# Performance work log

Hardware: AMD Instinct MI355X
Metric: run time of the kernel (lower is better)

The kernel has to match this reference:

```python
import jax, jax.numpy as jnp
import numpy as np

N_UP, N_DOWN, M, D, K, F, L, B = 16, 16, 4, 128, 64, 32, 3, 1024
N = N_UP + N_DOWN
H_W = 45  # round(sqrt(F*K)), hidden dim of the 2-layer w MLP
LOG2 = float(np.log(2.0))


def ssp(x):
    # shifted softplus activation used by deepqmc
    return jax.nn.softplus(x) - LOG2


def _pair_blocks(n_up, n_down):
    # replicate idx_perm(N,2) grouped by i, then idx_pair_spin partition
    n = n_up + n_down
    i = np.repeat(np.arange(n), n - 1)
    j = np.concatenate([np.concatenate([np.arange(k), np.arange(k + 1, n)]) for k in range(n)])
    blocks = []
    for mi, mj, ri, rj in [(True, True, n_up, max(n_up - 1, 0)),
                           (True, False, n_up, n_down),
                           (False, True, n_down, n_up),
                           (False, False, n_down, max(n_down - 1, 0))]:
        mask = ((i < n_up) == mi) & ((j < n_up) == mj)
        blocks.append((i[mask].reshape(ri, rj), j[mask].reshape(ri, rj)))
    return blocks

_BLOCKS = _pair_blocks(N_UP, N_DOWN)
_CHANS = [0, 1, 1, 0]  # same, anti, anti, same (w/g channel index; 2 = nuclear)


def setup_inputs() -> dict:
    key = jax.random.key(0)
    ks = jax.random.split(key, 12)
    s = 0.1
    return {
        'edges_elec': jax.random.normal(ks[0], (B, N, N, F), jnp.float32),
        'edges_nuc': jax.random.normal(ks[1], (B, N, M, F), jnp.float32),
        'X': jax.random.normal(ks[2], (1, D), jnp.float32) * s,
        'Y': jax.random.normal(ks[3], (M, K), jnp.float32) * s,
        'wW1': jax.random.normal(ks[4], (L, 3, H_W, F), jnp.float32) * s,
        'wb1': jax.random.normal(ks[5], (L, 3, H_W), jnp.float32) * s,
        'wW2': jax.random.normal(ks[6], (L, 3, K, H_W), jnp.float32) * s,
        'wb2': jax.random.normal(ks[7], (L, 3, K), jnp.float32) * s,
        'hW': jax.random.normal(ks[8], (L, K, D), jnp.float32) * s,
        'hb': jax.random.normal(ks[9], (L, K), jnp.float32) * s,
        'gW': jax.random.normal(ks[10], (L, 3, D, K), jnp.float32) * s,
        'gb': jax.random.normal(ks[11], (L, 3, D), jnp.float32) * s,
    }


def reference(edges_elec, edges_nuc, X, Y, wW1, wb1, wW2, wb2, hW, hb, gW, gb):
    def w_mlp(l, c, e):
        # 2-layer log-dim MLP: F -> H_W -> K with SSP in between
        return ssp(e @ wW1[l, c].T + wb1[l, c]) @ wW2[l, c].T + wb2[l, c]

    b = edges_nuc.shape[0]
    x = jnp.broadcast_to(X, (b, N, D))  # initial electron embeddings (n_up==n_down)
    for l in range(L):
        h = x @ hW[l].T + hb[l]  # shared h subnet: [b,N,K]
        zs = []
        for (ii, jj), c in zip(_BLOCKS, _CHANS):
            e = edges_elec[:, ii, jj, :]               # [b, ri, rj, F] gather
            msg = w_mlp(l, c, e) * h[:, jj, :]          # [b, ri, rj, K]
            zs.append(msg.sum(axis=-2))                 # segment-sum over j
        z_same = jnp.concatenate([zs[0], zs[3]], axis=-2)  # up then down
        z_anti = jnp.concatenate([zs[1], zs[2]], axis=-2)
        z_nuc = jnp.einsum('bnmk,mk->bnk', w_mlp(l, 2, edges_nuc), Y)
        update = (z_same @ gW[l, 0].T + gb[l, 0]
                  + z_anti @ gW[l, 1].T + gb[l, 1]
                  + z_nuc @ gW[l, 2].T + gb[l, 2])
        x = x + update  # resnet
    return x
```

## Files before the change

kernel.cpp:

```cpp
#include <hip/hip_runtime.h>
#include <math.h>

#define N_   32
#define NUP_ 16
#define M_   4
#define D_   128
#define K_   64
#define F_   32
#define H_   45
#define L_   3
#define LOG2_ 0.69314718055994530942f

typedef __attribute__((ext_vector_type(8))) short short8;
typedef __attribute__((ext_vector_type(4))) float float4v;

__device__ __forceinline__ float ssp(float v) {
    return __logf(1.0f + __expf(v)) - LOG2_;
}

__device__ __forceinline__ unsigned short f2bf(float x) {
    unsigned int u = __float_as_uint(x);
    return (unsigned short)((u + 0x7FFFu + ((u >> 16) & 1u)) >> 16);
}

__device__ __forceinline__ unsigned int pkbf(float x, float y) {
    return __builtin_amdgcn_perm(__float_as_uint(y) + 0x8000u,
                                 __float_as_uint(x) + 0x8000u, 0x07060302u);
}

__global__ __launch_bounds__(256) void prep_kernel(
    const float* __restrict__ wW1, const float* __restrict__ wb2_unused,
    const float* __restrict__ wW2, const float* __restrict__ wb2,
    const float* __restrict__ gW,  const float* __restrict__ hW,
    const float* __restrict__ gb,
    short* __restrict__ w1B, short* __restrict__ w2B,
    short* __restrict__ gB,  short* __restrict__ hB, float* __restrict__ gbs)
{
    int blk = blockIdx.x;
    int t = threadIdx.x;
    if (blk < 27) {
        int lc = blk / 3, nt = blk % 3;
        short* dst = w1B + (size_t)blk * 512;
        for (int idx = t; idx < 512; idx += 256) {
            int lane = idx >> 3, jj = idx & 7;
            int k = ((lane >> 4) << 3) + jj;
            int n = nt * 16 + (lane & 15);
            float v = (n < H_) ? wW1[((size_t)lc * H_ + n) * F_ + k] : 0.0f;
            dst[idx] = (short)f2bf(v);
        }
    } else if (blk < 99) {
        int b3 = blk - 27;
        int lc = b3 >> 3, rem = b3 & 7, ks = rem >> 2, nt = rem & 3;
        short* dst = w2B + (size_t)b3 * 512;
        for (int idx = t; idx < 512; idx += 256) {
            int lane = idx >> 3, jj = idx & 7;
            int p = ks * 32 + ((lane >> 4) << 3) + jj;
            int n = nt * 16 + (lane & 15);
            float v;
            if (p == 3) v = wb2[(size_t)lc * K_ + n];
            else if ((p & 3) < 3) {
                int u = (p & 3) * 16 + (p >> 2);
                v = (u < H_) ? wW2[((size_t)lc * K_ + n) * H_ + u] : 0.0f;
            } else v = 0.0f;
            dst[idx] = (short)f2bf(v);
        }
    } else if (blk < 243) {
        int g = blk - 99;
        int l = g / 48, rem = g % 48;
        short* dst = gB + (size_t)g * 512;
        for (int idx = t; idx < 512; idx += 256) {
            int lane = idx >> 3, jj = idx & 7;
            int k = (rem >> 3) * 32 + ((lane >> 4) << 3) + jj;
            int c = k >> 6, kk = k & 63;
            int n = ((rem & 7) * 16) + (lane & 15);
            dst[idx] = (short)f2bf(gW[(((size_t)l * 3 + c) * D_ + n) * K_ + kk]);
        }
    } else if (blk < 275) {
        int hh = blk - 243;
        int li = hh >> 4, rem = hh & 15;
        short* dst = hB + (size_t)hh * 512;
        for (int idx = t; idx < 512; idx += 256) {
            int lane = idx >> 3, jj = idx & 7;
            int p = (rem >> 2) * 32 + ((lane >> 4) << 3) + jj;
            int d = (p & 7) * 16 + (p >> 3);
            int n = ((rem & 3) * 16) + (lane & 15);
            dst[idx] = (short)f2bf(hW[(((size_t)(li + 1)) * K_ + n) * D_ + d]);
        }
    } else {
        for (int idx = t; idx < 384; idx += 256) {
            int l = idx >> 7, d = idx & 127;
            gbs[idx] = gb[((size_t)l * 3 + 0) * D_ + d]
                     + gb[((size_t)l * 3 + 1) * D_ + d]
                     + gb[((size_t)l * 3 + 2) * D_ + d];
        }
    }
}

__global__ __launch_bounds__(64) void h0_kernel(
    const float* __restrict__ X, const float* __restrict__ hW,
    const float* __restrict__ hb, float* __restrict__ h0)
{
    int k = threadIdx.x;
    float a = hb[k];
    const float* w = hW + (size_t)k * D_;
    #pragma unroll 8
    for (int dd = 0; dd < D_; ++dd) a += w[dd] * X[dd];
    h0[k] = a;
}

#define WSTRIDE 68
#define HDS 72
__global__ __launch_bounds__(256, 6) void edge_kernel(
    const float* __restrict__ ee, const float* __restrict__ en,
    const float* __restrict__ Y,
    const short* __restrict__ w1B, const float* __restrict__ wb1,
    const short* __restrict__ w2B,
    const float* __restrict__ h, const float* __restrict__ h0,
    unsigned short* __restrict__ zb, int l, int hmode)
{
    __shared__ float wrow[36 * WSTRIDE];
    __shared__ short hd_s[4][16 * HDS];

    const int tid  = threadIdx.x;
    const int wv   = tid >> 6;
    const int lane = tid & 63;
    const int quad = lane >> 4;
    const int l16  = lane & 15;
    const int b    = blockIdx.x >> 3;
    const int i    = ((blockIdx.x & 7) << 2) + wv;
    const int bi   = (b << 5) + i;

    {
        int row = tid >> 3;
        int col = (tid & 7) * 8;
        const float* src = hmode ? (h + ((size_t)(b * N_ + row)) * K_ + col) : (h0 + col);
        float4 v0 = *(const float4*)(src);
        float4 v1 = *(const float4*)(src + 4);
        *(float4*)(wrow + row * WSTRIDE + col)     = v0;
        *(float4*)(wrow + row * WSTRIDE + col + 4) = v1;
        if (tid < 32) {
            int r2 = tid >> 3, o2 = (tid & 7) * 8;
            float4 y0 = *(const float4*)(Y + (size_t)r2 * K_ + o2);
            float4 y1 = *(const float4*)(Y + (size_t)r2 * K_ + o2 + 4);
            *(float4*)(wrow + (32 + r2) * WSTRIDE + o2)     = y0;
            *(float4*)(wrow + (32 + r2) * WSTRIDE + o2 + 4) = y1;
        }
    }
    __syncthreads();

    const int cA = (i < NUP_) ? 0 : 1;
    short* hd = hd_s[wv];
    const unsigned int cpad = (l16 == 0) ? 0x3F808000u : 0u;

    #pragma unroll
    for (int t = 0; t < 3; ++t) {
        const int c  = (t == 2) ? 2 : ((t == 0) ? cA : 1 - cA);
        const int lc = l * 3 + c;

        float4 fa = {0.f, 0.f, 0.f, 0.f}, fb = {0.f, 0.f, 0.f, 0.f};
        if (t < 2) {
            const float* ep = ee + (((size_t)bi * N_) + t * 16 + l16) * F_ + quad * 8;
            fa = *(const float4*)(ep);
            fb = *(const float4*)(ep + 4);
        } else if (l16 < M_) {
            const float* np = en + (((size_t)bi * M_) + l16) * F_ + quad * 8;
            fa = *(const float4*)(np);
            fb = *(const float4*)(np + 4);
        }
        union { short8 s; unsigned int u[4]; } A;
        A.u[0] = pkbf(fa.x, fa.y); A.u[1] = pkbf(fa.z, fa.w);
        A.u[2] = pkbf(fb.x, fb.y); A.u[3] = pkbf(fb.z, fb.w);

        float4v acc1[3];
        #pragma unroll
        for (int nt = 0; nt < 3; ++nt) {
            int col = nt * 16 + l16;
            float b1c = (col < H_) ? wb1[(size_t)lc * H_ + col] : 0.0f;
            acc1[nt] = (float4v){b1c, b1c, b1c, b1c};
            short8 bf = *(const short8*)(w1B + (((size_t)lc * 3 + nt) << 9) + (lane << 3));
            acc1[nt] = __builtin_amdgcn_mfma_f32_16x16x32_bf16(A.s, bf, acc1[nt], 0, 0, 0);
        }

        #pragma unroll
        for (int r = 0; r < 4; ++r) {
            float s0 = ssp(acc1[0][r]);
            float s1 = ssp(acc1[1][r]);
            float s2 = ssp(acc1[2][r]);
            unsigned int lo = pkbf(s0, s1);
            unsigned int hi = __builtin_amdgcn_perm(cpad, __float_as_uint(s2) + 0x8000u, 0x07060302u);
            uint2 pr; pr.x = lo; pr.y = hi;
            *(uint2*)(hd + (quad * 4 + r) * HDS + 4 * l16) = pr;
        }

        float4v acc2[4];
        #pragma unroll
        for (int nt = 0; nt < 4; ++nt) acc2[nt] = (float4v){0.f, 0.f, 0.f, 0.f};
        #pragma unroll
        for (int ks = 0; ks < 2; ++ks) {
            short8 a2 = *(const short8*)(hd + l16 * HDS + ks * 32 + quad * 8);
            #pragma unroll
            for (int nt = 0; nt < 4; ++nt) {
                short8 bf = *(const short8*)(w2B + ((((size_t)lc * 2 + ks) * 4 + nt) << 9) + (lane << 3));
                acc2[nt] = __builtin_amdgcn_mfma_f32_16x16x32_bf16(a2, bf, acc2[nt], 0, 0, 0);
            }
        }

        float p0 = 0.f, p1 = 0.f, p2 = 0.f, p3 = 0.f;
        #pragma unroll
        for (int r = 0; r < 4; ++r) {
            int jrow = t * 16 + quad * 4 + r;
            const float* wr = wrow + jrow * WSTRIDE + l16;
            float w0 = wr[0], w1 = wr[16], w2 = wr[32], w3 = wr[48];
            bool live = (t == 2) ? (jrow < 36) : (jrow != i);
            if (!live) { w0 = 0.f; w1 = 0.f; w2 = 0.f; w3 = 0.f; }
            p0 += acc2[0][r] * w0;
            p1 += acc2[1][r] * w1;
            p2 += acc2[2][r] * w2;
            p3 += acc2[3][r] * w3;
        }
        p0 += __shfl_xor(p0, 16); p0 += __shfl_xor(p0, 32);
        p1 += __shfl_xor(p1, 16); p1 += __shfl_xor(p1, 32);
        p2 += __shfl_xor(p2, 16); p2 += __shfl_xor(p2, 32);
        p3 += __shfl_xor(p3, 16); p3 += __shfl_xor(p3, 32);

        float v = p0;
        v = (quad == 1) ? p1 : v;
        v = (quad == 2) ? p2 : v;
        v = (quad == 3) ? p3 : v;
        zb[(size_t)bi * 192 + c * 64 + lane] =
            (unsigned short)((__float_as_uint(v) + 0x8000u) >> 16);
    }
}

#define HXS 136
__global__ __launch_bounds__(256) void fuse_kernel(
    const unsigned short* __restrict__ zb, const short* __restrict__ gB,
    const float* __restrict__ gbs, const float* __restrict__ X,
    const short* __restrict__ hB, const float* __restrict__ hb,
    float* __restrict__ xout, float* __restrict__ hout,
    int l, int first, int compute_h)
{
    __shared__ short hx_s[4][16 * HXS];

    const int tid  = threadIdx.x;
    const int wv   = tid >> 6;
    const int lane = tid & 63;
    const int quad = lane >> 4;
    const int l16  = lane & 15;
    const int bi0  = (blockIdx.x * 4 + wv) * 16;

    float4v ax[8];
    #pragma unroll
    for (int nt = 0; nt < 8; ++nt) ax[nt] = (float4v){0.f, 0.f, 0.f, 0.f};
    const short* gb_ = gB + (size_t)l * 48 * 512;
    const short* zrow = (const short*)zb + ((size_t)(bi0 + l16)) * 192;
    #pragma unroll
    for (int ks = 0; ks < 6; ++ks) {
        short8 az = *(const short8*)(zrow + ks * 32 + quad * 8);
        #pragma unroll
        for (int nt = 0; nt < 8; ++nt) {
            short8 bf = *(const short8*)(gb_ + (((size_t)ks * 8 + nt) << 9) + (lane << 3));
            ax[nt] = __builtin_amdgcn_mfma_f32_16x16x32_bf16(az, bf, ax[nt], 0, 0, 0);
        }
    }

    float gv[8], xb[8];
    #pragma unroll
    for (int nt = 0; nt < 8; ++nt) {
        gv[nt] = gbs[(size_t)l * D_ + nt * 16 + l16];
        if (first) xb[nt] = X[nt * 16 + l16];
    }
    short* hx = hx_s[wv];
    #pragma unroll
    for (int r = 0; r < 4; ++r) {
        int row = quad * 4 + r;
        size_t gi = ((size_t)(bi0 + row)) * D_ + l16;
        float xv[8];
        #pragma unroll
        for (int nt = 0; nt < 8; ++nt) {
            float xo = (first ? xb[nt] : xout[gi + nt * 16]) + gv[nt] + ax[nt][r];
            xout[gi + nt * 16] = xo;
            xv[nt] = xo;
        }
        if (compute_h) {
            union { short8 s; unsigned int u[4]; } P;
            P.u[0] = pkbf(xv[0], xv[1]); P.u[1] = pkbf(xv[2], xv[3]);
            P.u[2] = pkbf(xv[4], xv[5]); P.u[3] = pkbf(xv[6], xv[7]);
            *(short8*)(hx + row * HXS + 8 * l16) = P.s;
        }
    }
    if (!compute_h) return;

    float4v ah[4];
    #pragma unroll
    for (int nt = 0; nt < 4; ++nt) ah[nt] = (float4v){0.f, 0.f, 0.f, 0.f};
    const short* hb_ = hB + (size_t)l * 16 * 512;
    #pragma unroll
    for (int ks = 0; ks < 4; ++ks) {
        short8 a = *(const short8*)(hx + l16 * HXS + ks * 32 + quad * 8);
        #pragma unroll
        for (int nt = 0; nt < 4; ++nt) {
            short8 bf = *(const short8*)(hb_ + (((size_t)ks * 4 + nt) << 9) + (lane << 3));
            ah[nt] = __builtin_amdgcn_mfma_f32_16x16x32_bf16(a, bf, ah[nt], 0, 0, 0);
        }
    }
    float hbv[4];
    #pragma unroll
    for (int nt = 0; nt < 4; ++nt) hbv[nt] = hb[((size_t)(l + 1)) * K_ + nt * 16 + l16];
    #pragma unroll
    for (int nt = 0; nt < 4; ++nt)
        #pragma unroll
        for (int r = 0; r < 4; ++r)
            hout[((size_t)(bi0 + quad * 4 + r)) * K_ + nt * 16 + l16] = ah[nt][r] + hbv[nt];
}

extern "C" void kernel_launch(void* const* d_in, const int* in_sizes, int n_in,
                              void* d_out, int out_size, void* d_ws, size_t ws_size,
                              hipStream_t stream)
{
    const float* ee  = (const float*)d_in[0];
    const float* en  = (const float*)d_in[1];
    const float* X   = (const float*)d_in[2];
    const float* Y   = (const float*)d_in[3];
    const float* wW1 = (const float*)d_in[4];
    const float* wb1 = (const float*)d_in[5];
    const float* wW2 = (const float*)d_in[6];
    const float* wb2 = (const float*)d_in[7];
    const float* hW  = (const float*)d_in[8];
    const float* hb  = (const float*)d_in[9];
    const float* gW  = (const float*)d_in[10];
    const float* gb  = (const float*)d_in[11];
    float* xout = (float*)d_out;

    char* ws = (char*)d_ws;
    float*          h   = (float*)(ws);
    unsigned short* zb  = (unsigned short*)(ws + 8388608);
    float*          h0  = (float*)(ws + 8388608 + 12582912);
    short*          w1B = (short*)(ws + 20971520 + 256);
    short*          w2B = w1B + (size_t)27 * 512;
    short*          gB  = w2B + (size_t)72 * 512;
    short*          hB  = gB  + (size_t)144 * 512;
    float*          gbs = (float*)(hB + (size_t)32 * 512);

    prep_kernel<<<276, 256, 0, stream>>>(wW1, wb1, wW2, wb2, gW, hW, gb,
                                         w1B, w2B, gB, hB, gbs);
    h0_kernel<<<1, 64, 0, stream>>>(X, hW, hb, h0);

    edge_kernel<<<8192, 256, 0, stream>>>(ee, en, Y, w1B, wb1, w2B, h, h0, zb, 0, 0);
    fuse_kernel<<<512, 256, 0, stream>>>(zb, gB, gbs, X, hB, hb, xout, h, 0, 1, 1);
    edge_kernel<<<8192, 256, 0, stream>>>(ee, en, Y, w1B, wb1, w2B, h, h0, zb, 1, 1);
    fuse_kernel<<<512, 256, 0, stream>>>(zb, gB, gbs, X, hB, hb, xout, h, 1, 0, 1);
    edge_kernel<<<8192, 256, 0, stream>>>(ee, en, Y, w1B, wb1, w2B, h, h0, zb, 2, 1);
    fuse_kernel<<<512, 256, 0, stream>>>(zb, gB, gbs, X, hB, hb, xout, h, 2, 0, 0);
}
```

Measured before the change: 438.9 us.

## Restructure edge and fuse kernels: larger blocks, LDS reductions, split-K fuse

The edge kernel now runs 512-thread blocks of eight electrons each. It preloads all edge features and biases up front, stores h/Y transposed so each lane reads them with one float4, and replaces the cross-quad shuffle reduction with a reduction through LDS. The fuse kernel moves from one 16-row tile per wave to one tile per block, with the 6 K-slices split across 3 waves and summed through shared memory before the resnet update and h MLP. The hW prep layout is simplified to match. The aim is to cut load latency, shuffle count and per-wave serial MFMA chains, at the cost of more LDS traffic, extra barriers and a relaxed wait-based reduction whose ordering correctness is fragile.

```diff
diff --git a/kernel.cpp b/kernel.cpp
--- a/kernel.cpp
+++ b/kernel.cpp
@@ -29,10 +29,9 @@
 }
 
 __global__ __launch_bounds__(256) void prep_kernel(
-    const float* __restrict__ wW1, const float* __restrict__ wb2_unused,
-    const float* __restrict__ wW2, const float* __restrict__ wb2,
-    const float* __restrict__ gW,  const float* __restrict__ hW,
-    const float* __restrict__ gb,
+    const float* __restrict__ wW1, const float* __restrict__ wW2,
+    const float* __restrict__ wb2, const float* __restrict__ gW,
+    const float* __restrict__ hW,  const float* __restrict__ gb,
     short* __restrict__ w1B, short* __restrict__ w2B,
     short* __restrict__ gB,  short* __restrict__ hB, float* __restrict__ gbs)
 {
@@ -81,8 +80,7 @@
         short* dst = hB + (size_t)hh * 512;
         for (int idx = t; idx < 512; idx += 256) {
             int lane = idx >> 3, jj = idx & 7;
-            int p = (rem >> 2) * 32 + ((lane >> 4) << 3) + jj;
-            int d = (p & 7) * 16 + (p >> 3);
+            int d = (rem >> 2) * 32 + ((lane >> 4) << 3) + jj;
             int n = ((rem & 3) * 16) + (lane & 15);
             dst[idx] = (short)f2bf(hW[(((size_t)(li + 1)) * K_ + n) * D_ + d]);
         }
@@ -108,9 +106,8 @@
     h0[k] = a;
 }
 
-#define WSTRIDE 68
 #define HDS 72
-__global__ __launch_bounds__(256, 6) void edge_kernel(
+__global__ __launch_bounds__(512, 5) void edge_kernel(
     const float* __restrict__ ee, const float* __restrict__ en,
     const float* __restrict__ Y,
     const short* __restrict__ w1B, const float* __restrict__ wb1,
@@ -118,67 +115,88 @@
     const float* __restrict__ h, const float* __restrict__ h0,
     unsigned short* __restrict__ zb, int l, int hmode)
 {
-    __shared__ float wrow[36 * WSTRIDE];
-    __shared__ short hd_s[4][16 * HDS];
+    __shared__ float wrowT[36 * 64];
+    __shared__ short hd_s[8][16 * HDS];
+    __shared__ float part_s[8][256];
 
     const int tid  = threadIdx.x;
     const int wv   = tid >> 6;
     const int lane = tid & 63;
     const int quad = lane >> 4;
     const int l16  = lane & 15;
-    const int b    = blockIdx.x >> 3;
-    const int i    = ((blockIdx.x & 7) << 2) + wv;
+    const int b    = blockIdx.x >> 2;
+    const int i    = ((blockIdx.x & 3) << 3) + wv;
     const int bi   = (b << 5) + i;
 
     {
-        int row = tid >> 3;
-        int col = (tid & 7) * 8;
-        const float* src = hmode ? (h + ((size_t)(b * N_ + row)) * K_ + col) : (h0 + col);
-        float4 v0 = *(const float4*)(src);
-        float4 v1 = *(const float4*)(src + 4);
-        *(float4*)(wrow + row * WSTRIDE + col)     = v0;
-        *(float4*)(wrow + row * WSTRIDE + col + 4) = v1;
-        if (tid < 32) {
-            int r2 = tid >> 3, o2 = (tid & 7) * 8;
-            float4 y0 = *(const float4*)(Y + (size_t)r2 * K_ + o2);
-            float4 y1 = *(const float4*)(Y + (size_t)r2 * K_ + o2 + 4);
-            *(float4*)(wrow + (32 + r2) * WSTRIDE + o2)     = y0;
-            *(float4*)(wrow + (32 + r2) * WSTRIDE + o2 + 4) = y1;
+        int row = tid >> 4;
+        int c0 = (tid & 15) * 4;
+        int m = c0 >> 4, lb = c0 & 15;
+        const float* src = hmode ? (h + ((size_t)(b * N_ + row)) * K_ + c0) : (h0 + c0);
+        float4 v = *(const float4*)src;
+        wrowT[row * 64 + (lb + 0) * 4 + m] = v.x;
+        wrowT[row * 64 + (lb + 1) * 4 + m] = v.y;
+        wrowT[row * 64 + (lb + 2) * 4 + m] = v.z;
+        wrowT[row * 64 + (lb + 3) * 4 + m] = v.w;
+        if (tid < 64) {
+            int r2 = 32 + (tid >> 4);
+            float4 y = *(const float4*)(Y + ((size_t)(tid >> 4)) * K_ + c0);
+            wrowT[r2 * 64 + (lb + 0) * 4 + m] = y.x;
+            wrowT[r2 * 64 + (lb + 1) * 4 + m] = y.y;
+            wrowT[r2 * 64 + (lb + 2) * 4 + m] = y.z;
+            wrowT[r2 * 64 + (lb + 3) * 4 + m] = y.w;
         }
     }
     __syncthreads();
 
     const int cA = (i < NUP_) ? 0 : 1;
+    const int cs0 = cA, cs1 = 1 - cA, cs2 = 2;
     short* hd = hd_s[wv];
+    float* part = part_s[wv];
     const unsigned int cpad = (l16 == 0) ? 0x3F808000u : 0u;
 
+    const float* ep = ee + (((size_t)bi * N_) + l16) * F_ + quad * 8;
+    float4 e0a = *(const float4*)(ep);
+    float4 e0b = *(const float4*)(ep + 4);
+    float4 e1a = *(const float4*)(ep + 16 * F_);
+    float4 e1b = *(const float4*)(ep + 16 * F_ + 4);
+    float4 e2a = {0.f,0.f,0.f,0.f}, e2b = {0.f,0.f,0.f,0.f};
+    if (l16 < M_) {
+        const float* np = en + (((size_t)bi * M_) + l16) * F_ + quad * 8;
+        e2a = *(const float4*)(np);
+        e2b = *(const float4*)(np + 4);
+    }
+    float b1r[9];
+    {
+        const int cls[3] = {l * 3 + cs0, l * 3 + cs1, l * 3 + cs2};
+        #pragma unroll
+        for (int t = 0; t < 3; ++t)
+            #pragma unroll
+            for (int nt = 0; nt < 3; ++nt) {
+                int col = nt * 16 + l16;
+                b1r[t * 3 + nt] = (col < H_) ? wb1[(size_t)cls[t] * H_ + col] : 0.0f;
+            }
+    }
+    union { short8 s; unsigned int u[4]; } A[3];
+    A[0].u[0] = pkbf(e0a.x, e0a.y); A[0].u[1] = pkbf(e0a.z, e0a.w);
+    A[0].u[2] = pkbf(e0b.x, e0b.y); A[0].u[3] = pkbf(e0b.z, e0b.w);
+    A[1].u[0] = pkbf(e1a.x, e1a.y); A[1].u[1] = pkbf(e1a.z, e1a.w);
+    A[1].u[2] = pkbf(e1b.x, e1b.y); A[1].u[3] = pkbf(e1b.z, e1b.w);
+    A[2].u[0] = pkbf(e2a.x, e2a.y); A[2].u[1] = pkbf(e2a.z, e2a.w);
+    A[2].u[2] = pkbf(e2b.x, e2b.y); A[2].u[3] = pkbf(e2b.z, e2b.w);
+
     #pragma unroll
     for (int t = 0; t < 3; ++t) {
-        const int c  = (t == 2) ? 2 : ((t == 0) ? cA : 1 - cA);
+        const int c  = (t == 0) ? cs0 : ((t == 1) ? cs1 : cs2);
         const int lc = l * 3 + c;
 
-        float4 fa = {0.f, 0.f, 0.f, 0.f}, fb = {0.f, 0.f, 0.f, 0.f};
-        if (t < 2) {
-            const float* ep = ee + (((size_t)bi * N_) + t * 16 + l16) * F_ + quad * 8;
-            fa = *(const float4*)(ep);
-            fb = *(const float4*)(ep + 4);
-        } else if (l16 < M_) {
-            const float* np = en + (((size_t)bi * M_) + l16) * F_ + quad * 8;
-            fa = *(const float4*)(np);
-            fb = *(const float4*)(np + 4);
-        }
-        union { short8 s; unsigned int u[4]; } A;
-        A.u[0] = pkbf(fa.x, fa.y); A.u[1] = pkbf(fa.z, fa.w);
-        A.u[2] = pkbf(fb.x, fb.y); A.u[3] = pkbf(fb.z, fb.w);
-
         float4v acc1[3];
         #pragma unroll
         for (int nt = 0; nt < 3; ++nt) {
-            int col = nt * 16 + l16;
-            float b1c = (col < H_) ? wb1[(size_t)lc * H_ + col] : 0.0f;
+            float b1c = b1r[t * 3 + nt];
             acc1[nt] = (float4v){b1c, b1c, b1c, b1c};
             short8 bf = *(const short8*)(w1B + (((size_t)lc * 3 + nt) << 9) + (lane << 3));
-            acc1[nt] = __builtin_amdgcn_mfma_f32_16x16x32_bf16(A.s, bf, acc1[nt], 0, 0, 0);
+            acc1[nt] = __builtin_amdgcn_mfma_f32_16x16x32_bf16(A[t].s, bf, acc1[nt], 0, 0, 0);
         }
 
         #pragma unroll
@@ -209,109 +227,131 @@
         #pragma unroll
         for (int r = 0; r < 4; ++r) {
             int jrow = t * 16 + quad * 4 + r;
-            const float* wr = wrow + jrow * WSTRIDE + l16;
-            float w0 = wr[0], w1 = wr[16], w2 = wr[32], w3 = wr[48];
+            int jcl = (jrow < 36) ? jrow : 35;
+            float4 wv4 = *(const float4*)(wrowT + jcl * 64 + l16 * 4);
             bool live = (t == 2) ? (jrow < 36) : (jrow != i);
-            if (!live) { w0 = 0.f; w1 = 0.f; w2 = 0.f; w3 = 0.f; }
-            p0 += acc2[0][r] * w0;
-            p1 += acc2[1][r] * w1;
-            p2 += acc2[2][r] * w2;
-            p3 += acc2[3][r] * w3;
-        }
-        p0 += __shfl_xor(p0, 16); p0 += __shfl_xor(p0, 32);
-        p1 += __shfl_xor(p1, 16); p1 += __shfl_xor(p1, 32);
-        p2 += __shfl_xor(p2, 16); p2 += __shfl_xor(p2, 32);
-        p3 += __shfl_xor(p3, 16); p3 += __shfl_xor(p3, 32);
-
-        float v = p0;
-        v = (quad == 1) ? p1 : v;
-        v = (quad == 2) ? p2 : v;
-        v = (quad == 3) ? p3 : v;
+            if (!live) { wv4.x = 0.f; wv4.y = 0.f; wv4.z = 0.f; wv4.w = 0.f; }
+            p0 += acc2[0][r] * wv4.x;
+            p1 += acc2[1][r] * wv4.y;
+            p2 += acc2[2][r] * wv4.z;
+            p3 += acc2[3][r] * wv4.w;
+        }
+        float4 pv; pv.x = p0; pv.y = p1; pv.z = p2; pv.w = p3;
+        *(float4*)(&part[(quad * 16 + l16) * 4]) = pv;
+        __builtin_amdgcn_s_waitcnt(0);
+        float zsum = part[l16 * 4 + quad] + part[64 + l16 * 4 + quad]
+                   + part[128 + l16 * 4 + quad] + part[192 + l16 * 4 + quad];
         zb[(size_t)bi * 192 + c * 64 + lane] =
-            (unsigned short)((__float_as_uint(v) + 0x8000u) >> 16);
-    }
-}
-
+            (unsigned short)((__float_as_uint(zsum) + 0x8000u) >> 16);
+    }
+}
+
+#define XPS 132
 #define HXS 136
-__global__ __launch_bounds__(256) void fuse_kernel(
+__global__ __launch_bounds__(192, 4) void fuse_kernel(
     const unsigned short* __restrict__ zb, const short* __restrict__ gB,
     const float* __restrict__ gbs, const float* __restrict__ X,
     const short* __restrict__ hB, const float* __restrict__ hb,
     float* __restrict__ xout, float* __restrict__ hout,
     int l, int first, int compute_h)
 {
-    __shared__ short hx_s[4][16 * HXS];
+    __shared__ float xpart[3][16 * XPS];
+    __shared__ short hx[16 * HXS];
 
     const int tid  = threadIdx.x;
     const int wv   = tid >> 6;
     const int lane = tid & 63;
     const int quad = lane >> 4;
     const int l16  = lane & 15;
-    const int bi0  = (blockIdx.x * 4 + wv) * 16;
+    const int bi0  = blockIdx.x * 16;
 
     float4v ax[8];
     #pragma unroll
     for (int nt = 0; nt < 8; ++nt) ax[nt] = (float4v){0.f, 0.f, 0.f, 0.f};
-    const short* gb_ = gB + (size_t)l * 48 * 512;
     const short* zrow = (const short*)zb + ((size_t)(bi0 + l16)) * 192;
-    #pragma unroll
-    for (int ks = 0; ks < 6; ++ks) {
+    const short* gl = gB + (size_t)l * 48 * 512;
+    #pragma unroll
+    for (int ks2 = 0; ks2 < 2; ++ks2) {
+        int ks = wv * 2 + ks2;
         short8 az = *(const short8*)(zrow + ks * 32 + quad * 8);
         #pragma unroll
         for (int nt = 0; nt < 8; ++nt) {
-            short8 bf = *(const short8*)(gb_ + (((size_t)ks * 8 + nt) << 9) + (lane << 3));
+            short8 bf = *(const short8*)(gl + (((size_t)ks * 8 + nt) << 9) + (lane << 3));
             ax[nt] = __builtin_amdgcn_mfma_f32_16x16x32_bf16(az, bf, ax[nt], 0, 0, 0);
         }
     }
-
-    float gv[8], xb[8];
-    #pragma unroll
-    for (int nt = 0; nt < 8; ++nt) {
-        gv[nt] = gbs[(size_t)l * D_ + nt * 16 + l16];
-        if (first) xb[nt] = X[nt * 16 + l16];
-    }
-    short* hx = hx_s[wv];
+    float* xp = xpart[wv];
     #pragma unroll
     for (int r = 0; r < 4; ++r) {
         int row = quad * 4 + r;
-        size_t gi = ((size_t)(bi0 + row)) * D_ + l16;
-        float xv[8];
-        #pragma unroll
-        for (int nt = 0; nt < 8; ++nt) {
-            float xo = (first ? xb[nt] : xout[gi + nt * 16]) + gv[nt] + ax[nt][r];
-            xout[gi + nt * 16] = xo;
-            xv[nt] = xo;
+        float4 lo; lo.x = ax[0][r]; lo.y = ax[1][r]; lo.z = ax[2][r]; lo.w = ax[3][r];
+        float4 hi; hi.x = ax[4][r]; hi.y = ax[5][r]; hi.z = ax[6][r]; hi.w = ax[7][r];
+        *(float4*)(&xp[row * XPS + l16 * 8])     = lo;
+        *(float4*)(&xp[row * XPS + l16 * 8 + 4]) = hi;
+    }
+    __syncthreads();
+
+    if (tid < 128) {
+        int row = tid >> 3, nt = tid & 7;
+        int dbase = nt * 16;
+        size_t gi = ((size_t)(bi0 + row)) * D_ + dbase;
+        float acc[16];
+        #pragma unroll
+        for (int j = 0; j < 16; ++j) {
+            int o = row * XPS + j * 8 + nt;
+            acc[j] = xpart[0][o] + xpart[1][o] + xpart[2][o];
+        }
+        float res[16];
+        #pragma unroll
+        for (int q = 0; q < 4; ++q) {
+            float4 rv = first ? *(const float4*)(X + dbase + q * 4)
+                              : *(const float4*)(xout + gi + q * 4);
+            float4 gv = *(const float4*)(gbs + (size_t)l * D_ + dbase + q * 4);
+            res[q*4+0] = rv.x + gv.x; res[q*4+1] = rv.y + gv.y;
+            res[q*4+2] = rv.z + gv.z; res[q*4+3] = rv.w + gv.w;
+        }
+        float xo[16];
+        #pragma unroll
+        for (int j = 0; j < 16; ++j) xo[j] = acc[j] + res[j];
+        #pragma unroll
+        for (int q = 0; q < 4; ++q) {
+            float4 sv; sv.x = xo[q*4+0]; sv.y = xo[q*4+1]; sv.z = xo[q*4+2]; sv.w = xo[q*4+3];
+            *(float4*)(xout + gi + q * 4) = sv;
         }
         if (compute_h) {
-            union { short8 s; unsigned int u[4]; } P;
-            P.u[0] = pkbf(xv[0], xv[1]); P.u[1] = pkbf(xv[2], xv[3]);
-            P.u[2] = pkbf(xv[4], xv[5]); P.u[3] = pkbf(xv[6], xv[7]);
-            *(short8*)(hx + row * HXS + 8 * l16) = P.s;
+            union { short8 s; unsigned int u[4]; } P0, P1;
+            P0.u[0] = pkbf(xo[0], xo[1]);  P0.u[1] = pkbf(xo[2], xo[3]);
+            P0.u[2] = pkbf(xo[4], xo[5]);  P0.u[3] = pkbf(xo[6], xo[7]);
+            P1.u[0] = pkbf(xo[8], xo[9]);  P1.u[1] = pkbf(xo[10], xo[11]);
+            P1.u[2] = pkbf(xo[12], xo[13]); P1.u[3] = pkbf(xo[14], xo[15]);
+            *(short8*)(hx + row * HXS + dbase)     = P0.s;
+            *(short8*)(hx + row * HXS + dbase + 8) = P1.s;
         }
     }
     if (!compute_h) return;
+    __syncthreads();
 
     float4v ah[4];
     #pragma unroll
     for (int nt = 0; nt < 4; ++nt) ah[nt] = (float4v){0.f, 0.f, 0.f, 0.f};
-    const short* hb_ = hB + (size_t)l * 16 * 512;
+    const short* hl = hB + (size_t)l * 16 * 512;
     #pragma unroll
     for (int ks = 0; ks < 4; ++ks) {
         short8 a = *(const short8*)(hx + l16 * HXS + ks * 32 + quad * 8);
         #pragma unroll
         for (int nt = 0; nt < 4; ++nt) {
-            short8 bf = *(const short8*)(hb_ + (((size_t)ks * 4 + nt) << 9) + (lane << 3));
+            short8 bf = *(const short8*)(hl + (((size_t)ks * 4 + nt) << 9) + (lane << 3));
             ah[nt] = __builtin_amdgcn_mfma_f32_16x16x32_bf16(a, bf, ah[nt], 0, 0, 0);
         }
     }
-    float hbv[4];
-    #pragma unroll
-    for (int nt = 0; nt < 4; ++nt) hbv[nt] = hb[((size_t)(l + 1)) * K_ + nt * 16 + l16];
-    #pragma unroll
-    for (int nt = 0; nt < 4; ++nt)
+    int nlo = (wv == 0) ? 0 : ((wv == 1) ? 2 : 3);
+    int nhi = (wv == 0) ? 2 : (nlo + 1);
+    for (int nt = nlo; nt < nhi; ++nt) {
+        float hbv = hb[((size_t)(l + 1)) * K_ + nt * 16 + l16];
         #pragma unroll
         for (int r = 0; r < 4; ++r)
-            hout[((size_t)(bi0 + quad * 4 + r)) * K_ + nt * 16 + l16] = ah[nt][r] + hbv[nt];
+            hout[((size_t)(bi0 + quad * 4 + r)) * K_ + nt * 16 + l16] = ah[nt][r] + hbv;
+    }
 }
 
 extern "C" void kernel_launch(void* const* d_in, const int* in_sizes, int n_in,
@@ -342,14 +382,14 @@
     short*          hB  = gB  + (size_t)144 * 512;
     float*          gbs = (float*)(hB + (size_t)32 * 512);
 
-    prep_kernel<<<276, 256, 0, stream>>>(wW1, wb1, wW2, wb2, gW, hW, gb,
+    prep_kernel<<<276, 256, 0, stream>>>(wW1, wW2, wb2, gW, hW, gb,
                                          w1B, w2B, gB, hB, gbs);
     h0_kernel<<<1, 64, 0, stream>>>(X, hW, hb, h0);
 
-    edge_kernel<<<8192, 256, 0, stream>>>(ee, en, Y, w1B, wb1, w2B, h, h0, zb, 0, 0);
-    fuse_kernel<<<512, 256, 0, stream>>>(zb, gB, gbs, X, hB, hb, xout, h, 0, 1, 1);
-    edge_kernel<<<8192, 256, 0, stream>>>(ee, en, Y, w1B, wb1, w2B, h, h0, zb, 1, 1);
-    fuse_kernel<<<512, 256, 0, stream>>>(zb, gB, gbs, X, hB, hb, xout, h, 1, 0, 1);
-    edge_kernel<<<8192, 256, 0, stream>>>(ee, en, Y, w1B, wb1, w2B, h, h0, zb, 2, 1);
-    fuse_kernel<<<512, 256, 0, stream>>>(zb, gB, gbs, X, hB, hb, xout, h, 2, 0, 0);
-}
+    edge_kernel<<<4096, 512, 0, stream>>>(ee, en, Y, w1B, wb1, w2B, h, h0, zb, 0, 0);
+    fuse_kernel<<<2048, 192, 0, stream>>>(zb, gB, gbs, X, hB, hb, xout, h, 0, 1, 1);
+    edge_kernel<<<4096, 512, 0, stream>>>(ee, en, Y, w1B, wb1, w2B, h, h0, zb, 1, 1);
+    fuse_kernel<<<2048, 192, 0, stream>>>(zb, gB, gbs, X, hB, hb, xout, h, 1, 0, 1);
+    edge_kernel<<<4096, 512, 0, stream>>>(ee, en, Y, w1B, wb1, w2B, h, h0, zb, 2, 1);
+    fuse_kernel<<<2048, 192, 0, stream>>>(zb, gB, gbs, X, hB, hb, xout, h, 2, 0, 0);
+}
```

Result: slower. 452.7 us (+3.1%).
